# Optimization experiments

Hardware: AMD Instinct MI355X
Metric: run time of the kernel (lower is better)

## Reference

```python
import jax, jax.numpy as jnp
import numpy as np

B, HH, WW, C, HEADS = 8, 56, 56, 384, 6
DIM_OUT = 384


def _upsample2x_bilinear(x):
    # x: [..., m, n] -> [..., 2m, 2n]; matches torch F.interpolate bilinear align_corners=False
    m, n = x.shape[-2], x.shape[-1]
    def coords(inn):
        c = (jnp.arange(2 * inn) + 0.5) / 2.0 - 0.5
        c = jnp.clip(c, 0.0, inn - 1)
        i0 = jnp.floor(c).astype(jnp.int32)
        i1 = jnp.minimum(i0 + 1, inn - 1)
        return i0, i1, (c - i0).astype(x.dtype)
    i0, i1, wy = coords(m)
    j0, j1, wx = coords(n)
    rows = x[..., i0, :] * (1 - wy)[:, None] + x[..., i1, :] * wy[:, None]
    return rows[..., :, j0] * (1 - wx) + rows[..., :, j1] * wx


def setup_inputs() -> dict:
    key = jax.random.key(0)
    ks = jax.random.split(key, 12)
    inp = {
        'x': jax.random.normal(ks[0], (B, HH * WW, C), jnp.float32),
        'res_attn': jax.random.normal(ks[1], (B, HEADS, (HH // 4) * (WW // 4), (HH // 2) * (WW // 2)), jnp.float32),
        'conv_q_w': jax.random.normal(ks[2], (C, 1, 3, 3), jnp.float32) * 0.05,
        'ln_g': jnp.ones((C,), jnp.float32),
        'ln_b': jnp.zeros((C,), jnp.float32),
        'wq': jax.random.normal(ks[3], (DIM_OUT, C), jnp.float32) * 0.02,
        'wk': jax.random.normal(ks[4], (DIM_OUT, C), jnp.float32) * 0.02,
        'wv': jax.random.normal(ks[5], (DIM_OUT, C), jnp.float32) * 0.02,
        'w_proj': jax.random.normal(ks[6], (DIM_OUT, DIM_OUT), jnp.float32) * 0.02,
        'b_proj': jnp.zeros((DIM_OUT,), jnp.float32),
        'w_fuse': jax.random.normal(ks[7], (HEADS, 2 * HEADS, 1, 1), jnp.float32) * 0.1,
        'b_fuse': jnp.zeros((HEADS,), jnp.float32),
        'h': HH,
        'w': WW,
    }
    return inp


def reference(x, res_attn, conv_q_w, ln_g, ln_b, wq, wk, wv, w_proj, b_proj, w_fuse, b_fuse, h, w):
    Bz, _, Cc = x.shape
    heads = w_fuse.shape[0]
    xi = x.transpose(0, 2, 1).reshape(Bz, Cc, h, w)  # b c h w
    # conv_proj_q: depthwise conv k3 s2 p1 (no bias), then LayerNorm
    q = jax.lax.conv_general_dilated(
        xi, conv_q_w, (2, 2), ((1, 1), (1, 1)),
        dimension_numbers=('NCHW', 'OIHW', 'NCHW'), feature_group_count=Cc)
    hq, wq2 = q.shape[2], q.shape[3]
    q = q.reshape(Bz, Cc, hq * wq2).transpose(0, 2, 1)  # b t c
    mu = q.mean(-1, keepdims=True)
    var = ((q - mu) ** 2).mean(-1, keepdims=True)
    q = (q - mu) / jnp.sqrt(var + 1e-5) * ln_g + ln_b
    # conv_proj_k/v: avg pool k2 s2 p0
    kv = xi.reshape(Bz, Cc, h // 2, 2, w // 2, 2).mean(axis=(3, 5))
    kv = kv.reshape(Bz, Cc, (h // 2) * (w // 2)).transpose(0, 2, 1)  # b t c
    dim_out = wq.shape[0]
    dh = dim_out // heads
    def split(t):
        return t.reshape(Bz, t.shape[1], heads, dh).transpose(0, 2, 1, 3)
    qh = split(q @ wq.T)
    kh = split(kv @ wk.T)
    vh = split(kv @ wv.T)
    scale = dim_out ** -0.5
    attn_score = jnp.einsum('bhlk,bhtk->bhlt', qh, kh) * scale  # [B,H,L,T]
    sh, sw = h // 4, w // 4
    a = res_attn.shape[-1]
    rx = res_attn[:, :, :sh * sw, :]
    rx = rx.reshape(Bz * heads, sh * sw, a).transpose(0, 2, 1).reshape(Bz * heads, a, sh, sw)
    rx = _upsample2x_bilinear(rx)  # (b h) a 2sh 2sw
    rx = rx.reshape(Bz, heads, a, 4 * sh * sw).transpose(0, 1, 3, 2)  # b h L a
    cat = jnp.concatenate([attn_score, rx], axis=1)  # [B, 2H, L, T]
    attn_score = jnp.einsum('bclt,oc->bolt', cat, w_fuse[:, :, 0, 0]) + b_fuse[None, :, None, None]
    attn = jax.nn.softmax(attn_score, axis=-1)
    out = jnp.einsum('bhlt,bhtv->bhlv', attn, vh)
    out = out.transpose(0, 2, 1, 3).reshape(Bz, -1, dim_out)
    return out @ w_proj.T + b_proj
```

## Files before the change

kernel.cpp:

```cpp
#include <hip/hip_runtime.h>

typedef unsigned int uint;
typedef unsigned short ushort_t;
typedef short bf16x8 __attribute__((ext_vector_type(8)));
typedef float f32x4 __attribute__((ext_vector_type(4)));

__device__ __forceinline__ ushort_t f2bf(float f) {
  uint u = __builtin_bit_cast(uint, f);
  u += 0x7fffu + ((u >> 16) & 1u);
  return (ushort_t)(u >> 16);
}
__device__ __forceinline__ float bf2f(ushort_t s) {
  return __builtin_bit_cast(float, (uint)s << 16);
}
__device__ __forceinline__ bf16x8 ld_frag(const ushort_t* p) {
  return __builtin_bit_cast(bf16x8, *(const uint4*)p);
}

__global__ __launch_bounds__(384) void k_convln(
    const float* __restrict__ x, const float* __restrict__ wc,
    const float* __restrict__ g, const float* __restrict__ bb,
    ushort_t* __restrict__ qout)
{
  const int b  = blockIdx.x / 784;
  const int t  = blockIdx.x % 784;
  const int oy = t / 28, ox = t % 28;
  const int c  = threadIdx.x;
  const float* xb = x + (size_t)b * 3136 * 384 + c;
  float acc = 0.f;
  #pragma unroll
  for (int ky = 0; ky < 3; ky++) {
    const int iy = 2 * oy - 1 + ky;
    if (iy < 0 || iy >= 56) continue;
    #pragma unroll
    for (int kx = 0; kx < 3; kx++) {
      const int ix = 2 * ox - 1 + kx;
      if (ix < 0 || ix >= 56) continue;
      acc += wc[c * 9 + ky * 3 + kx] * xb[(size_t)(iy * 56 + ix) * 384];
    }
  }
  float s = acc, s2 = acc * acc;
  #pragma unroll
  for (int off = 32; off >= 1; off >>= 1) {
    s  += __shfl_xor(s,  off);
    s2 += __shfl_xor(s2, off);
  }
  __shared__ float ps[6], ps2[6];
  if ((c & 63) == 0) { ps[c >> 6] = s; ps2[c >> 6] = s2; }
  __syncthreads();
  float S = 0.f, S2 = 0.f;
  #pragma unroll
  for (int i = 0; i < 6; i++) { S += ps[i]; S2 += ps2[i]; }
  const float mu  = S * (1.f / 384.f);
  const float var = S2 * (1.f / 384.f) - mu * mu;
  const float inv = rsqrtf(var + 1e-5f);
  qout[((size_t)b * 784 + t) * 384 + c] = f2bf((acc - mu) * inv * g[c] + bb[c]);
}

__global__ __launch_bounds__(256) void k_pool(
    const float* __restrict__ x, ushort_t* __restrict__ kvout)
{
  const int idx = blockIdx.x * 256 + threadIdx.x;
  const int c = idx % 384;
  const int t = (idx / 384) % 784;
  const int b = idx / (384 * 784);
  const int ty = t / 28, tx = t % 28;
  const float* xb = x + (size_t)b * 3136 * 384 + c;
  const int r0 = (2 * ty) * 56 + 2 * tx;
  const float v = xb[(size_t)r0 * 384] + xb[(size_t)(r0 + 1) * 384]
                + xb[(size_t)(r0 + 56) * 384] + xb[(size_t)(r0 + 57) * 384];
  kvout[idx] = f2bf(v * 0.25f);
}

__global__ __launch_bounds__(256) void k_wcvt(
    const float* __restrict__ a, const float* __restrict__ b,
    const float* __restrict__ c, const float* __restrict__ d,
    ushort_t* __restrict__ oa, ushort_t* __restrict__ ob,
    ushort_t* __restrict__ oc, ushort_t* __restrict__ od)
{
  const int i = blockIdx.x * 256 + threadIdx.x;
  if (i < 147456) {
    oa[i] = f2bf(a[i]); ob[i] = f2bf(b[i]);
    oc[i] = f2bf(c[i]); od[i] = f2bf(d[i]);
  }
}

template<int MODE>
__global__ __launch_bounds__(256) void k_gemm(
    const ushort_t* __restrict__ X, const ushort_t* __restrict__ W,
    const float* __restrict__ bias, void* __restrict__ Y)
{
  __shared__ ushort_t As[128][40];
  __shared__ ushort_t Bs[128][40];
  const int tid = threadIdx.x, w = tid >> 6, lane = tid & 63;
  const int quad = lane >> 4, r = lane & 15;
  const int m0 = blockIdx.y * 128, n0 = blockIdx.x * 128;
  const int wm = w >> 1, wn = w & 1;
  const int lr = tid >> 2, lc = (tid & 3) << 3;
  const ushort_t* xp = X + (size_t)(m0 + lr) * 384 + lc;
  const ushort_t* wp = W + (size_t)(n0 + lr) * 384 + lc;
  f32x4 acc[4][4] = {};
  for (int k0 = 0; k0 < 384; k0 += 32) {
    __syncthreads();
    *(uint4*)&As[lr][lc]      = *(const uint4*)(xp + k0);
    *(uint4*)&As[lr + 64][lc] = *(const uint4*)(xp + (size_t)64 * 384 + k0);
    *(uint4*)&Bs[lr][lc]      = *(const uint4*)(wp + k0);
    *(uint4*)&Bs[lr + 64][lc] = *(const uint4*)(wp + (size_t)64 * 384 + k0);
    __syncthreads();
    bf16x8 af[4], bf_[4];
    #pragma unroll
    for (int mt = 0; mt < 4; mt++) af[mt]  = *(const bf16x8*)&As[wm * 64 + mt * 16 + r][quad * 8];
    #pragma unroll
    for (int nt = 0; nt < 4; nt++) bf_[nt] = *(const bf16x8*)&Bs[wn * 64 + nt * 16 + r][quad * 8];
    #pragma unroll
    for (int mt = 0; mt < 4; mt++)
      #pragma unroll
      for (int nt = 0; nt < 4; nt++)
        acc[mt][nt] = __builtin_amdgcn_mfma_f32_16x16x32_bf16(af[mt], bf_[nt], acc[mt][nt], 0, 0, 0);
  }
  #pragma unroll
  for (int mt = 0; mt < 4; mt++) {
    #pragma unroll
    for (int nt = 0; nt < 4; nt++) {
      #pragma unroll
      for (int i = 0; i < 4; i++) {
        const int row = m0 + wm * 64 + mt * 16 + quad * 4 + i;
        const int col = n0 + wn * 64 + nt * 16 + r;
        const float v = acc[mt][nt][i];
        if constexpr (MODE == 2) {
          ((float*)Y)[(size_t)row * 384 + col] = v + bias[col];
        } else if constexpr (MODE == 0) {
          ((ushort_t*)Y)[(size_t)row * 384 + col] = f2bf(v);
        } else {
          const int bb = row / 784, tt = row % 784;
          ((ushort_t*)Y)[((size_t)bb * 384 + col) * 784 + tt] = f2bf(v);
        }
      }
    }
  }
}

__global__ __launch_bounds__(256) void k_qk(
    const ushort_t* __restrict__ Qb, const ushort_t* __restrict__ Kb,
    ushort_t* __restrict__ S)
{
  const int tid = threadIdx.x, w = tid >> 6, lane = tid & 63;
  const int quad = lane >> 4, r = lane & 15;
  const int bh = blockIdx.z, b = bh / 6, h = bh % 6;
  const int m0 = blockIdx.y * 64 + w * 16;
  const int t0 = blockIdx.x * 112;
  const int lq = min(m0 + r, 783);
  const ushort_t* qp = Qb + (size_t)(b * 784 + lq) * 384 + h * 64 + quad * 8;
  const bf16x8 a0 = ld_frag(qp), a1 = ld_frag(qp + 32);
  f32x4 acc[7] = {};
  #pragma unroll
  for (int j = 0; j < 7; j++) {
    const int t = t0 + j * 16 + r;
    const ushort_t* kp = Kb + (size_t)(b * 784 + t) * 384 + h * 64 + quad * 8;
    acc[j] = __builtin_amdgcn_mfma_f32_16x16x32_bf16(a0, ld_frag(kp),      acc[j], 0, 0, 0);
    acc[j] = __builtin_amdgcn_mfma_f32_16x16x32_bf16(a1, ld_frag(kp + 32), acc[j], 0, 0, 0);
  }
  const float scale = 0.05103103630798288f;
  #pragma unroll
  for (int j = 0; j < 7; j++) {
    #pragma unroll
    for (int i = 0; i < 4; i++) {
      const int lo = m0 + quad * 4 + i;
      if (lo < 784)
        S[((size_t)(b * 784 + lo) * 6 + h) * 784 + t0 + j * 16 + r] = f2bf(acc[j][i] * scale);
    }
  }
}

__global__ __launch_bounds__(256) void k_fuse(
    ushort_t* __restrict__ S, const float* __restrict__ ra,
    const float* __restrict__ w_fuse, const float* __restrict__ b_fuse)
{
  const int tid = threadIdx.x;
  const int bl = blockIdx.x, b = bl / 784, l = bl % 784;
  __shared__ float wf[72], bfu[6];
  __shared__ float redm[4][6], reds[4][6];
  if (tid < 72) wf[tid] = w_fuse[tid];
  if (tid < 6)  bfu[tid] = b_fuse[tid];
  __syncthreads();

  const int Y = l / 28, X = l % 28;
  const float cy = fminf(fmaxf((float)Y * 0.5f - 0.25f, 0.f), 13.f);
  const float cx = fminf(fmaxf((float)X * 0.5f - 0.25f, 0.f), 13.f);
  const int y0 = (int)cy, y1 = min(y0 + 1, 13);
  const int x0 = (int)cx, x1 = min(x0 + 1, 13);
  const float fy = cy - (float)y0, fx = cx - (float)x0;
  const float w00 = (1.f - fy) * (1.f - fx), w01 = (1.f - fy) * fx;
  const float w10 = fy * (1.f - fx),         w11 = fy * fx;
  const int p00 = (y0 * 14 + x0) * 784, p01 = (y0 * 14 + x1) * 784;
  const int p10 = (y1 * 14 + x0) * 784, p11 = (y1 * 14 + x1) * 784;

  ushort_t* Srow = S + (size_t)bl * 6 * 784;
  const float* rab = ra + (size_t)b * 6 * 196 * 784;

  float F[4][6];
  #pragma unroll
  for (int j = 0; j < 4; j++) {
    const int t = tid + j * 256;
    if (t < 784) {
      float a[6];
      #pragma unroll
      for (int o = 0; o < 6; o++) a[o] = bfu[o];
      #pragma unroll
      for (int c = 0; c < 6; c++) {
        const float* rc = rab + (size_t)c * (196 * 784);
        const float rx = w00 * rc[p00 + t] + w01 * rc[p01 + t]
                       + w10 * rc[p10 + t] + w11 * rc[p11 + t];
        const float sv = bf2f(Srow[c * 784 + t]);
        #pragma unroll
        for (int o = 0; o < 6; o++) a[o] += wf[o * 12 + c] * sv + wf[o * 12 + 6 + c] * rx;
      }
      #pragma unroll
      for (int o = 0; o < 6; o++) F[j][o] = a[o];
    } else {
      #pragma unroll
      for (int o = 0; o < 6; o++) F[j][o] = -1e30f;
    }
  }
  float mx[6];
  #pragma unroll
  for (int o = 0; o < 6; o++) {
    mx[o] = fmaxf(fmaxf(F[0][o], F[1][o]), fmaxf(F[2][o], F[3][o]));
    #pragma unroll
    for (int off = 32; off >= 1; off >>= 1) mx[o] = fmaxf(mx[o], __shfl_xor(mx[o], off));
  }
  if ((tid & 63) == 0) {
    #pragma unroll
    for (int o = 0; o < 6; o++) redm[tid >> 6][o] = mx[o];
  }
  __syncthreads();
  float M[6];
  #pragma unroll
  for (int o = 0; o < 6; o++)
    M[o] = fmaxf(fmaxf(redm[0][o], redm[1][o]), fmaxf(redm[2][o], redm[3][o]));
  float sm[6] = {};
  #pragma unroll
  for (int j = 0; j < 4; j++)
    #pragma unroll
    for (int o = 0; o < 6; o++) {
      const float p = __expf(F[j][o] - M[o]);
      F[j][o] = p; sm[o] += p;
    }
  #pragma unroll
  for (int o = 0; o < 6; o++) {
    #pragma unroll
    for (int off = 32; off >= 1; off >>= 1) sm[o] += __shfl_xor(sm[o], off);
  }
  if ((tid & 63) == 0) {
    #pragma unroll
    for (int o = 0; o < 6; o++) reds[tid >> 6][o] = sm[o];
  }
  __syncthreads();
  float inv[6];
  #pragma unroll
  for (int o = 0; o < 6; o++)
    inv[o] = 1.f / (reds[0][o] + reds[1][o] + reds[2][o] + reds[3][o]);
  #pragma unroll
  for (int j = 0; j < 4; j++) {
    const int t = tid + j * 256;
    if (t < 784) {
      #pragma unroll
      for (int o = 0; o < 6; o++) Srow[o * 784 + t] = f2bf(F[j][o] * inv[o]);
    }
  }
}

__global__ __launch_bounds__(256) void k_pv(
    const ushort_t* __restrict__ P, const ushort_t* __restrict__ Vt,
    ushort_t* __restrict__ O)
{
  const int tid = threadIdx.x, w = tid >> 6, lane = tid & 63;
  const int quad = lane >> 4, r = lane & 15;
  const int bo = blockIdx.y, b = bo / 6, o = bo % 6;
  const int m0 = blockIdx.x * 64 + w * 16;
  const int lq = min(m0 + r, 783);
  const ushort_t* ap = P + ((size_t)(b * 784 + lq) * 6 + o) * 784 + quad * 8;
  const ushort_t* bp = Vt + ((size_t)b * 384 + o * 64 + r) * 784 + quad * 8;
  f32x4 acc[4] = {};
  for (int kk = 0; kk < 25; kk++) {
    const int k0 = kk * 32;
    const bool full = (kk < 24) | (quad < 2);
    bf16x8 af = {}, bf_[4] = {};
    if (full) {
      af = ld_frag(ap + k0);
      #pragma unroll
      for (int nt = 0; nt < 4; nt++) bf_[nt] = ld_frag(bp + (size_t)nt * 16 * 784 + k0);
    }
    #pragma unroll
    for (int nt = 0; nt < 4; nt++)
      acc[nt] = __builtin_amdgcn_mfma_f32_16x16x32_bf16(af, bf_[nt], acc[nt], 0, 0, 0);
  }
  #pragma unroll
  for (int nt = 0; nt < 4; nt++) {
    #pragma unroll
    for (int i = 0; i < 4; i++) {
      const int lo = m0 + quad * 4 + i;
      if (lo < 784)
        O[(size_t)(b * 784 + lo) * 384 + o * 64 + nt * 16 + r] = f2bf(acc[nt][i]);
    }
  }
}

extern "C" void kernel_launch(void* const* d_in, const int* in_sizes, int n_in,
                              void* d_out, int out_size, void* d_ws, size_t ws_size,
                              hipStream_t stream)
{
  const float* x        = (const float*)d_in[0];
  const float* res_attn = (const float*)d_in[1];
  const float* conv_w   = (const float*)d_in[2];
  const float* ln_g     = (const float*)d_in[3];
  const float* ln_b     = (const float*)d_in[4];
  const float* wq       = (const float*)d_in[5];
  const float* wk       = (const float*)d_in[6];
  const float* wv       = (const float*)d_in[7];
  const float* w_proj   = (const float*)d_in[8];
  const float* b_proj   = (const float*)d_in[9];
  const float* w_fuse   = (const float*)d_in[10];
  const float* b_fuse   = (const float*)d_in[11];
  float* out = (float*)d_out;

  const size_t NE = (size_t)8 * 784 * 384;
  const size_t NW = 147456;
  ushort_t* q_ln_b = (ushort_t*)d_ws;
  ushort_t* kv_b   = q_ln_b + NE;
  ushort_t* Qb     = kv_b + NE;
  ushort_t* Kb     = Qb + NE;
  ushort_t* Vt     = Kb + NE;
  ushort_t* Opre   = Vt + NE;
  ushort_t* wqb    = Opre + NE;
  ushort_t* wkb    = wqb + NW;
  ushort_t* wvb    = wkb + NW;
  ushort_t* wpb    = wvb + NW;
  ushort_t* S      = wpb + NW;

  k_convln<<<dim3(8 * 784), dim3(384), 0, stream>>>(x, conv_w, ln_g, ln_b, q_ln_b);
  k_pool  <<<dim3(9408),    dim3(256), 0, stream>>>(x, kv_b);
  k_wcvt  <<<dim3(576),     dim3(256), 0, stream>>>(wq, wk, wv, w_proj, wqb, wkb, wvb, wpb);

  k_gemm<0><<<dim3(3, 49), dim3(256), 0, stream>>>(q_ln_b, wqb, nullptr, Qb);
  k_gemm<0><<<dim3(3, 49), dim3(256), 0, stream>>>(kv_b,   wkb, nullptr, Kb);
  k_gemm<1><<<dim3(3, 49), dim3(256), 0, stream>>>(kv_b,   wvb, nullptr, Vt);

  k_qk  <<<dim3(7, 13, 48), dim3(256), 0, stream>>>(Qb, Kb, S);
  k_fuse<<<dim3(8 * 784),   dim3(256), 0, stream>>>(S, res_attn, w_fuse, b_fuse);
  k_pv  <<<dim3(13, 48),    dim3(256), 0, stream>>>(S, Vt, Opre);

  k_gemm<2><<<dim3(3, 49), dim3(256), 0, stream>>>(Opre, wpb, b_proj, out);
}
```

Baseline: 329.6 us.

## Fuse QK, residual-attention fuse, softmax and PV into one flash-style kernel

Replaces the three-kernel attention path (score GEMM, head-mixing fuse with bilinear residual and softmax, then PV GEMM) with a single kernel using online softmax over 64-key tiles. Each block handles 16 query rows across all 6 heads, computes the scores into shared memory, mixes heads with the upsampled residual attention, and accumulates P·V with rescaling. The aim is to avoid writing and re-reading the large bf16 score/probability tensor in global memory. In exchange the grid is only 392 blocks with per-tile syncs, and K/V fragments are loaded straight from global memory without sharing.

After: 401.5 us. 21.8% more time.

```diff
diff --git a/kernel.cpp b/kernel.cpp
--- a/kernel.cpp
+++ b/kernel.cpp
@@ -140,53 +140,40 @@
   }
 }
 
-__global__ __launch_bounds__(256) void k_qk(
+__global__ __launch_bounds__(256) void k_fattn(
     const ushort_t* __restrict__ Qb, const ushort_t* __restrict__ Kb,
-    ushort_t* __restrict__ S)
-{
-  const int tid = threadIdx.x, w = tid >> 6, lane = tid & 63;
+    const ushort_t* __restrict__ Vt, const float* __restrict__ ra,
+    const float* __restrict__ w_fuse, const float* __restrict__ b_fuse,
+    ushort_t* __restrict__ O)
+{
+  __shared__ float    Ssc[6][16][68];
+  __shared__ ushort_t Pl[6][16][72];
+  __shared__ float m_st[6][16], s_st[6][16], a_st[6][16];
+  __shared__ float wf[72], bfu[6];
+
+  const int tid  = threadIdx.x;
+  const int w    = tid >> 6, lane = tid & 63;
   const int quad = lane >> 4, r = lane & 15;
-  const int bh = blockIdx.z, b = bh / 6, h = bh % 6;
-  const int m0 = blockIdx.y * 64 + w * 16;
-  const int t0 = blockIdx.x * 112;
-  const int lq = min(m0 + r, 783);
-  const ushort_t* qp = Qb + (size_t)(b * 784 + lq) * 384 + h * 64 + quad * 8;
-  const bf16x8 a0 = ld_frag(qp), a1 = ld_frag(qp + 32);
-  f32x4 acc[7] = {};
-  #pragma unroll
-  for (int j = 0; j < 7; j++) {
-    const int t = t0 + j * 16 + r;
-    const ushort_t* kp = Kb + (size_t)(b * 784 + t) * 384 + h * 64 + quad * 8;
-    acc[j] = __builtin_amdgcn_mfma_f32_16x16x32_bf16(a0, ld_frag(kp),      acc[j], 0, 0, 0);
-    acc[j] = __builtin_amdgcn_mfma_f32_16x16x32_bf16(a1, ld_frag(kp + 32), acc[j], 0, 0, 0);
-  }
-  const float scale = 0.05103103630798288f;
-  #pragma unroll
-  for (int j = 0; j < 7; j++) {
-    #pragma unroll
-    for (int i = 0; i < 4; i++) {
-      const int lo = m0 + quad * 4 + i;
-      if (lo < 784)
-        S[((size_t)(b * 784 + lo) * 6 + h) * 784 + t0 + j * 16 + r] = f2bf(acc[j][i] * scale);
-    }
-  }
-}
-
-__global__ __launch_bounds__(256) void k_fuse(
-    ushort_t* __restrict__ S, const float* __restrict__ ra,
-    const float* __restrict__ w_fuse, const float* __restrict__ b_fuse)
-{
-  const int tid = threadIdx.x;
-  const int bl = blockIdx.x, b = bl / 784, l = bl % 784;
-  __shared__ float wf[72], bfu[6];
-  __shared__ float redm[4][6], reds[4][6];
+  const int b    = blockIdx.x & 7;
+  const int m0   = (blockIdx.x >> 3) * 16;
+
   if (tid < 72) wf[tid] = w_fuse[tid];
   if (tid < 6)  bfu[tid] = b_fuse[tid];
-  __syncthreads();
-
-  const int Y = l / 28, X = l % 28;
-  const float cy = fminf(fmaxf((float)Y * 0.5f - 0.25f, 0.f), 13.f);
-  const float cx = fminf(fmaxf((float)X * 0.5f - 0.25f, 0.f), 13.f);
+  if (tid < 96) { (&m_st[0][0])[tid] = -1e30f; (&s_st[0][0])[tid] = 0.f; }
+
+  const ushort_t* qrow = Qb + ((size_t)(b * 784 + m0 + r)) * 384 + quad * 8;
+  bf16x8 qf[6][2];
+  #pragma unroll
+  for (int h = 0; h < 6; h++) {
+    qf[h][0] = ld_frag(qrow + h * 64);
+    qf[h][1] = ld_frag(qrow + h * 64 + 32);
+  }
+
+  const int bl_l = tid >> 4, tq = tid & 15;
+  const int L = m0 + bl_l;
+  const int Yc = L / 28, Xc = L % 28;
+  const float cy = fminf(fmaxf((float)Yc * 0.5f - 0.25f, 0.f), 13.f);
+  const float cx = fminf(fmaxf((float)Xc * 0.5f - 0.25f, 0.f), 13.f);
   const int y0 = (int)cy, y1 = min(y0 + 1, 13);
   const int x0 = (int)cx, x1 = min(x0 + 1, 13);
   const float fy = cy - (float)y0, fx = cx - (float)x0;
@@ -194,114 +181,115 @@
   const float w10 = fy * (1.f - fx),         w11 = fy * fx;
   const int p00 = (y0 * 14 + x0) * 784, p01 = (y0 * 14 + x1) * 784;
   const int p10 = (y1 * 14 + x0) * 784, p11 = (y1 * 14 + x1) * 784;
-
-  ushort_t* Srow = S + (size_t)bl * 6 * 784;
   const float* rab = ra + (size_t)b * 6 * 196 * 784;
 
-  float F[4][6];
-  #pragma unroll
-  for (int j = 0; j < 4; j++) {
-    const int t = tid + j * 256;
-    if (t < 784) {
-      float a[6];
-      #pragma unroll
-      for (int o = 0; o < 6; o++) a[o] = bfu[o];
+  const size_t kbase  = (size_t)b * 784 * 384;
+  const size_t vtbase = (size_t)b * 384 * 784;
+  const float scale = 0.05103103630798288f;
+
+  f32x4 oacc[6] = {};
+
+  for (int it = 0; it < 13; it++) {
+    const int t0 = it * 64;
+
+    {
+      const int tA = min(t0 + w * 16 + r, 783);
+      const ushort_t* krow = Kb + kbase + (size_t)tA * 384 + quad * 8;
+      #pragma unroll
+      for (int h = 0; h < 6; h++) {
+        f32x4 sc = {};
+        sc = __builtin_amdgcn_mfma_f32_16x16x32_bf16(qf[h][0], ld_frag(krow + h * 64),      sc, 0, 0, 0);
+        sc = __builtin_amdgcn_mfma_f32_16x16x32_bf16(qf[h][1], ld_frag(krow + h * 64 + 32), sc, 0, 0, 0);
+        #pragma unroll
+        for (int i = 0; i < 4; i++)
+          Ssc[h][quad * 4 + i][w * 16 + r] = sc[i] * scale;
+      }
+    }
+    __syncthreads();
+
+    {
+      const int t4  = t0 + tq * 4;
+      const int t4c = min(t4, 780);
+      float4 sv[6], rx[6];
+      #pragma unroll
+      for (int c = 0; c < 6; c++) sv[c] = *(const float4*)&Ssc[c][bl_l][tq * 4];
       #pragma unroll
       for (int c = 0; c < 6; c++) {
-        const float* rc = rab + (size_t)c * (196 * 784);
-        const float rx = w00 * rc[p00 + t] + w01 * rc[p01 + t]
-                       + w10 * rc[p10 + t] + w11 * rc[p11 + t];
-        const float sv = bf2f(Srow[c * 784 + t]);
+        const float* rc = rab + (size_t)c * 153664 + t4c;
+        const float4 a = *(const float4*)(rc + p00);
+        const float4 bq = *(const float4*)(rc + p01);
+        const float4 cc = *(const float4*)(rc + p10);
+        const float4 d = *(const float4*)(rc + p11);
+        rx[c].x = w00 * a.x + w01 * bq.x + w10 * cc.x + w11 * d.x;
+        rx[c].y = w00 * a.y + w01 * bq.y + w10 * cc.y + w11 * d.y;
+        rx[c].z = w00 * a.z + w01 * bq.z + w10 * cc.z + w11 * d.z;
+        rx[c].w = w00 * a.w + w01 * bq.w + w10 * cc.w + w11 * d.w;
+      }
+      float F[6][4];
+      #pragma unroll
+      for (int o = 0; o < 6; o++) {
+        float4 acc4 = {bfu[o], bfu[o], bfu[o], bfu[o]};
         #pragma unroll
-        for (int o = 0; o < 6; o++) a[o] += wf[o * 12 + c] * sv + wf[o * 12 + 6 + c] * rx;
-      }
-      #pragma unroll
-      for (int o = 0; o < 6; o++) F[j][o] = a[o];
-    } else {
-      #pragma unroll
-      for (int o = 0; o < 6; o++) F[j][o] = -1e30f;
-    }
-  }
-  float mx[6];
+        for (int c = 0; c < 6; c++) {
+          const float w1 = wf[o * 12 + c], w2 = wf[o * 12 + 6 + c];
+          acc4.x += w1 * sv[c].x + w2 * rx[c].x;
+          acc4.y += w1 * sv[c].y + w2 * rx[c].y;
+          acc4.z += w1 * sv[c].z + w2 * rx[c].z;
+          acc4.w += w1 * sv[c].w + w2 * rx[c].w;
+        }
+        F[o][0] = acc4.x; F[o][1] = acc4.y; F[o][2] = acc4.z; F[o][3] = acc4.w;
+      }
+      #pragma unroll
+      for (int j = 0; j < 4; j++) {
+        if (t4 + j >= 784) {
+          #pragma unroll
+          for (int o = 0; o < 6; o++) F[o][j] = -1e30f;
+        }
+      }
+      #pragma unroll
+      for (int o = 0; o < 6; o++) {
+        float mx = fmaxf(fmaxf(F[o][0], F[o][1]), fmaxf(F[o][2], F[o][3]));
+        #pragma unroll
+        for (int off = 8; off >= 1; off >>= 1) mx = fmaxf(mx, __shfl_xor(mx, off));
+        const float m_old = m_st[o][bl_l];
+        const float nm = fmaxf(m_old, mx);
+        const float al = __expf(m_old - nm);
+        float p0 = __expf(F[o][0] - nm), p1 = __expf(F[o][1] - nm);
+        float p2 = __expf(F[o][2] - nm), p3 = __expf(F[o][3] - nm);
+        float sm = p0 + p1 + p2 + p3;
+        #pragma unroll
+        for (int off = 8; off >= 1; off >>= 1) sm += __shfl_xor(sm, off);
+        const uint lo = (uint)f2bf(p0) | ((uint)f2bf(p1) << 16);
+        const uint hi = (uint)f2bf(p2) | ((uint)f2bf(p3) << 16);
+        *(uint2*)&Pl[o][bl_l][tq * 4] = uint2{lo, hi};
+        if (tq == 0) {
+          m_st[o][bl_l] = nm;
+          s_st[o][bl_l] = s_st[o][bl_l] * al + sm;
+          a_st[o][bl_l] = al;
+        }
+      }
+    }
+    __syncthreads();
+
+    #pragma unroll
+    for (int o = 0; o < 6; o++) {
+      const f32x4 al4 = *(const f32x4*)&a_st[o][quad * 4];
+      oacc[o] *= al4;
+      const bf16x8 pa0 = *(const bf16x8*)&Pl[o][r][quad * 8];
+      const bf16x8 pa1 = *(const bf16x8*)&Pl[o][r][quad * 8 + 32];
+      const ushort_t* vrow = Vt + vtbase + (size_t)(o * 64 + w * 16 + r) * 784 + t0 + quad * 8;
+      oacc[o] = __builtin_amdgcn_mfma_f32_16x16x32_bf16(pa0, ld_frag(vrow),      oacc[o], 0, 0, 0);
+      oacc[o] = __builtin_amdgcn_mfma_f32_16x16x32_bf16(pa1, ld_frag(vrow + 32), oacc[o], 0, 0, 0);
+    }
+  }
+
   #pragma unroll
   for (int o = 0; o < 6; o++) {
-    mx[o] = fmaxf(fmaxf(F[0][o], F[1][o]), fmaxf(F[2][o], F[3][o]));
-    #pragma unroll
-    for (int off = 32; off >= 1; off >>= 1) mx[o] = fmaxf(mx[o], __shfl_xor(mx[o], off));
-  }
-  if ((tid & 63) == 0) {
-    #pragma unroll
-    for (int o = 0; o < 6; o++) redm[tid >> 6][o] = mx[o];
-  }
-  __syncthreads();
-  float M[6];
-  #pragma unroll
-  for (int o = 0; o < 6; o++)
-    M[o] = fmaxf(fmaxf(redm[0][o], redm[1][o]), fmaxf(redm[2][o], redm[3][o]));
-  float sm[6] = {};
-  #pragma unroll
-  for (int j = 0; j < 4; j++)
-    #pragma unroll
-    for (int o = 0; o < 6; o++) {
-      const float p = __expf(F[j][o] - M[o]);
-      F[j][o] = p; sm[o] += p;
-    }
-  #pragma unroll
-  for (int o = 0; o < 6; o++) {
-    #pragma unroll
-    for (int off = 32; off >= 1; off >>= 1) sm[o] += __shfl_xor(sm[o], off);
-  }
-  if ((tid & 63) == 0) {
-    #pragma unroll
-    for (int o = 0; o < 6; o++) reds[tid >> 6][o] = sm[o];
-  }
-  __syncthreads();
-  float inv[6];
-  #pragma unroll
-  for (int o = 0; o < 6; o++)
-    inv[o] = 1.f / (reds[0][o] + reds[1][o] + reds[2][o] + reds[3][o]);
-  #pragma unroll
-  for (int j = 0; j < 4; j++) {
-    const int t = tid + j * 256;
-    if (t < 784) {
-      #pragma unroll
-      for (int o = 0; o < 6; o++) Srow[o * 784 + t] = f2bf(F[j][o] * inv[o]);
-    }
-  }
-}
-
-__global__ __launch_bounds__(256) void k_pv(
-    const ushort_t* __restrict__ P, const ushort_t* __restrict__ Vt,
-    ushort_t* __restrict__ O)
-{
-  const int tid = threadIdx.x, w = tid >> 6, lane = tid & 63;
-  const int quad = lane >> 4, r = lane & 15;
-  const int bo = blockIdx.y, b = bo / 6, o = bo % 6;
-  const int m0 = blockIdx.x * 64 + w * 16;
-  const int lq = min(m0 + r, 783);
-  const ushort_t* ap = P + ((size_t)(b * 784 + lq) * 6 + o) * 784 + quad * 8;
-  const ushort_t* bp = Vt + ((size_t)b * 384 + o * 64 + r) * 784 + quad * 8;
-  f32x4 acc[4] = {};
-  for (int kk = 0; kk < 25; kk++) {
-    const int k0 = kk * 32;
-    const bool full = (kk < 24) | (quad < 2);
-    bf16x8 af = {}, bf_[4] = {};
-    if (full) {
-      af = ld_frag(ap + k0);
-      #pragma unroll
-      for (int nt = 0; nt < 4; nt++) bf_[nt] = ld_frag(bp + (size_t)nt * 16 * 784 + k0);
-    }
-    #pragma unroll
-    for (int nt = 0; nt < 4; nt++)
-      acc[nt] = __builtin_amdgcn_mfma_f32_16x16x32_bf16(af, bf_[nt], acc[nt], 0, 0, 0);
-  }
-  #pragma unroll
-  for (int nt = 0; nt < 4; nt++) {
+    const f32x4 s4 = *(const f32x4*)&s_st[o][quad * 4];
     #pragma unroll
     for (int i = 0; i < 4; i++) {
-      const int lo = m0 + quad * 4 + i;
-      if (lo < 784)
-        O[(size_t)(b * 784 + lo) * 384 + o * 64 + nt * 16 + r] = f2bf(acc[nt][i]);
+      const int row = b * 784 + m0 + quad * 4 + i;
+      O[(size_t)row * 384 + o * 64 + w * 16 + r] = f2bf(oacc[o][i] / s4[i]);
     }
   }
 }
@@ -336,7 +324,6 @@
   ushort_t* wkb    = wqb + NW;
   ushort_t* wvb    = wkb + NW;
   ushort_t* wpb    = wvb + NW;
-  ushort_t* S      = wpb + NW;
 
   k_convln<<<dim3(8 * 784), dim3(384), 0, stream>>>(x, conv_w, ln_g, ln_b, q_ln_b);
   k_pool  <<<dim3(9408),    dim3(256), 0, stream>>>(x, kv_b);
@@ -346,9 +333,7 @@
   k_gemm<0><<<dim3(3, 49), dim3(256), 0, stream>>>(kv_b,   wkb, nullptr, Kb);
   k_gemm<1><<<dim3(3, 49), dim3(256), 0, stream>>>(kv_b,   wvb, nullptr, Vt);
 
-  k_qk  <<<dim3(7, 13, 48), dim3(256), 0, stream>>>(Qb, Kb, S);
-  k_fuse<<<dim3(8 * 784),   dim3(256), 0, stream>>>(S, res_attn, w_fuse, b_fuse);
-  k_pv  <<<dim3(13, 48),    dim3(256), 0, stream>>>(S, Vt, Opre);
+  k_fattn<<<dim3(392), dim3(256), 0, stream>>>(Qb, Kb, Vt, res_attn, w_fuse, b_fuse, Opre);
 
   k_gemm<2><<<dim3(3, 49), dim3(256), 0, stream>>>(Opre, wpb, b_proj, out);
 }
```
